# Optimization experiments

Hardware: AMD Instinct MI355X
Metric: run time of the kernel (lower is better)

## Reference

```python
import jax, jax.numpy as jnp
import numpy as np

B, L, D, H = 4, 2048, 1024, 16
HD = D // H  # head_dim = 64


def setup_inputs() -> dict:
    key = jax.random.key(0)
    ks = jax.random.split(key, 13)
    s = 1.0 / np.sqrt(D)
    inp = {
        'q': jax.random.normal(ks[0], (B, L, D), jnp.float32),
        'k': jax.random.normal(ks[1], (B, L, D), jnp.float32),
        'v': jax.random.normal(ks[2], (B, L, D), jnp.float32),
        'mask': jax.random.randint(ks[3], (B, 1, L, L), 0, 2, jnp.int32),
        'WQ': jax.random.normal(ks[4], (D, D), jnp.float32) * s,
        'bQ': jnp.zeros((D,), jnp.float32),
        'WK': jax.random.normal(ks[5], (D, D), jnp.float32) * s,
        'bK': jnp.zeros((D,), jnp.float32),
        'WV': jax.random.normal(ks[6], (D, D), jnp.float32) * s,
        'bV': jnp.zeros((D,), jnp.float32),
        'WO': jax.random.normal(ks[7], (D, D), jnp.float32) * s,
        'bO': jnp.zeros((D,), jnp.float32),
    }
    return inp


def reference(q, k, v, mask, WQ, bQ, WK, bK, WV, bV, WO, bO):
    # Linear projections (torch Linear: x @ W.T + b; here W stored as [D,D], use x @ W + b equivalently)
    Q = q @ WQ + bQ  # [B, L, D]
    K = k @ WK + bK
    V = v @ WV + bV
    # split heads -> [B, H, L, HD]
    Q = Q.reshape(B, L, H, HD).transpose(0, 2, 1, 3)
    K = K.reshape(B, L, H, HD).transpose(0, 2, 1, 3)
    V = V.reshape(B, L, H, HD).transpose(0, 2, 1, 3)
    scale = 1.0 / np.sqrt(HD).astype(np.float32)
    scores = jnp.einsum('bhqd,bhkd->bhqk', Q, K) * scale  # [B, H, Lq, Lk]
    scores = jnp.where(mask == 0, -jnp.inf, scores)  # mask broadcasts over heads
    attn = jax.nn.softmax(scores, axis=-1)
    # dropout p=0 (eval) -> identity
    ctx = jnp.einsum('bhqk,bhkd->bhqd', attn, V)  # [B, H, L, HD]
    ctx = ctx.transpose(0, 2, 1, 3).reshape(B, L, D)
    return ctx @ WO + bO
```

## Files before the change

kernel.cpp:

```cpp
#include <hip/hip_runtime.h>
#include <math.h>

#define B_  4
#define L_  2048
#define D_  1024
#define H_  16
#define HD_ 64

typedef __attribute__((ext_vector_type(8))) short short8;
typedef __attribute__((ext_vector_type(4))) float f32x4;

__device__ static inline unsigned short f2bf(float f) {
    union { float f; unsigned int u; } v; v.f = f;
    const unsigned int u = v.u;
    return (unsigned short)((u + 0x7FFFu + ((u >> 16) & 1u)) >> 16);
}

__device__ static inline void async_copy16(const void* g, void* lds)
{
    __builtin_amdgcn_global_load_lds(
        (const __attribute__((address_space(1))) void*)g,
        (__attribute__((address_space(3))) void*)lds, 16, 0, 0);
}

__global__ __launch_bounds__(256) void cvt_bf16_kernel(
    const float* __restrict__ in, unsigned short* __restrict__ out)
{
    const size_t i = ((size_t)blockIdx.x * 256 + threadIdx.x) * 8;
    const float4 x = *(const float4*)&in[i];
    const float4 y = *(const float4*)&in[i + 4];
    ushort4 o0, o1;
    o0.x = f2bf(x.x); o0.y = f2bf(x.y); o0.z = f2bf(x.z); o0.w = f2bf(x.w);
    o1.x = f2bf(y.x); o1.y = f2bf(y.y); o1.z = f2bf(y.z); o1.w = f2bf(y.w);
    *(ushort4*)&out[i]     = o0;
    *(ushort4*)&out[i + 4] = o1;
}

__global__ __launch_bounds__(256) void transpose_bf16_kernel(
    const float* __restrict__ W, unsigned short* __restrict__ WT)
{
    __shared__ float t[32][33];
    const int c  = threadIdx.x & 31;
    const int r8 = threadIdx.x >> 5;
    const int k0 = blockIdx.y * 32;
    const int n0 = blockIdx.x * 32;
    #pragma unroll
    for (int i = 0; i < 4; ++i) {
        const int r = r8 + i * 8;
        t[r][c] = W[(size_t)(k0 + r) * 1024 + n0 + c];
    }
    __syncthreads();
    #pragma unroll
    for (int i = 0; i < 4; ++i) {
        const int r = r8 + i * 8;
        WT[(size_t)(n0 + r) * 1024 + k0 + c] = f2bf(t[c][r]);
    }
}

__global__ __launch_bounds__(256) void vtrans_kernel(
    const float* __restrict__ Vp, unsigned short* __restrict__ vtb)
{
    __shared__ float t[64][65];
    const int tid = threadIdx.x;
    const int l0  = blockIdx.x * 64;
    const int h   = blockIdx.y;
    const int b   = blockIdx.z;
    const int rr  = tid >> 4;
    const int c4  = (tid & 15) * 4;
    #pragma unroll
    for (int i = 0; i < 4; ++i) {
        const int r = i * 16 + rr;
        const float4 x = *(const float4*)&Vp[((size_t)(b * L_ + l0 + r)) * D_ + h * 64 + c4];
        t[r][c4] = x.x; t[r][c4 + 1] = x.y; t[r][c4 + 2] = x.z; t[r][c4 + 3] = x.w;
    }
    __syncthreads();
    #pragma unroll
    for (int i = 0; i < 4; ++i) {
        const int d = i * 16 + rr;
        ushort4 o;
        o.x = f2bf(t[c4 + 0][d]); o.y = f2bf(t[c4 + 1][d]);
        o.z = f2bf(t[c4 + 2][d]); o.w = f2bf(t[c4 + 3][d]);
        *(ushort4*)&vtb[((size_t)((b * H_ + h) * 64 + d)) * L_ + l0 + c4] = o;
    }
}

__global__ __launch_bounds__(256) void pack_mask_t_kernel(
    const int* __restrict__ mask, unsigned int* __restrict__ mbt)
{
    const unsigned g = blockIdx.x * 256 + threadIdx.x;
    const int v = mask[g];
    const unsigned long long bm = __ballot(v != 0);
    const int lane = threadIdx.x & 63;
    const int b = g >> 22;
    const int q = (g >> 11) & 2047;
    const int k = g & 2047;
    const unsigned idx = ((unsigned)(b * 32 + (k >> 6)) * 2048 + q) * 2 + ((k >> 5) & 1);
    if (lane == 0)       mbt[idx] = (unsigned)bm;
    else if (lane == 32) mbt[idx] = (unsigned)(bm >> 32);
}

__global__ __launch_bounds__(256) void gemm_mfma_kernel(
    const unsigned short* __restrict__ A, const unsigned short* __restrict__ WT,
    const float* __restrict__ bias, float* __restrict__ C,
    int M, int N, int K)
{
    __shared__ __align__(16) unsigned short At[128 * 64];
    __shared__ __align__(16) unsigned short Bt[128 * 64];

    const int tid  = threadIdx.x;
    const int lane = tid & 63;
    const int wave = tid >> 6;
    const int wm   = wave >> 1;
    const int wn   = wave & 1;
    const int quad = lane >> 4;
    const int l15  = lane & 15;
    const int m0   = blockIdx.y * 128;
    const int n0   = blockIdx.x * 128;

    f32x4 acc[4][4];
    #pragma unroll
    for (int i = 0; i < 4; ++i)
        #pragma unroll
        for (int j = 0; j < 4; ++j) acc[i][j] = (f32x4)0.f;

    for (int k0 = 0; k0 < K; k0 += 64) {
        __syncthreads();
        #pragma unroll
        for (int i = 0; i < 4; ++i) {
            const int fb  = i * 256 + wave * 64;
            const int f   = fb + lane;
            const int row = f >> 3;
            const int c8  = f & 7;
            async_copy16(&A [(size_t)(m0 + row) * K + k0 + c8 * 8],
                         (char*)At + (size_t)fb * 16);
            async_copy16(&WT[(size_t)(n0 + row) * K + k0 + c8 * 8],
                         (char*)Bt + (size_t)fb * 16);
        }
        __syncthreads();

        #pragma unroll
        for (int kk = 0; kk < 64; kk += 32) {
            short8 afr[4], bfr[4];
            #pragma unroll
            for (int mt = 0; mt < 4; ++mt)
                afr[mt] = *(const short8*)&At[(size_t)(wm * 64 + mt * 16 + l15) * 64 + kk + quad * 8];
            #pragma unroll
            for (int nt = 0; nt < 4; ++nt)
                bfr[nt] = *(const short8*)&Bt[(size_t)(wn * 64 + nt * 16 + l15) * 64 + kk + quad * 8];
            #pragma unroll
            for (int mt = 0; mt < 4; ++mt)
                #pragma unroll
                for (int nt = 0; nt < 4; ++nt)
                    acc[mt][nt] = __builtin_amdgcn_mfma_f32_16x16x32_bf16(
                        afr[mt], bfr[nt], acc[mt][nt], 0, 0, 0);
        }
    }

    #pragma unroll
    for (int nt = 0; nt < 4; ++nt) {
        const int col = n0 + wn * 64 + nt * 16 + l15;
        const float bv = bias[col];
        #pragma unroll
        for (int mt = 0; mt < 4; ++mt) {
            const int r0 = m0 + wm * 64 + mt * 16 + quad * 4;
            #pragma unroll
            for (int r = 0; r < 4; ++r)
                C[(size_t)(r0 + r) * N + col] = acc[mt][nt][r] + bv;
        }
    }
}

#define AQ 128
#define AK 64
#define PSTR 72

__global__ __launch_bounds__(256) void attn_mfma_kernel(
    const unsigned short* __restrict__ Qb,
    const unsigned short* __restrict__ Kb,
    const unsigned short* __restrict__ Vtg,
    const unsigned int* __restrict__ mbt,
    unsigned short* __restrict__ Cb)
{
    __shared__ __align__(16) unsigned short Kt[AK * 64];
    __shared__ __align__(16) unsigned short Vs[64 * AK];
    __shared__ __align__(16) unsigned short Pt[AQ * PSTR];
    __shared__ __align__(16) unsigned long long Mt[AQ];

    const int tid  = threadIdx.x;
    const int lane = tid & 63;
    const int w    = tid >> 6;
    const int quad = lane >> 4;
    const int l15  = lane & 15;
    const int q0   = blockIdx.x * AQ;
    const int h    = blockIdx.y;
    const int b    = blockIdx.z;

    const float scale = 0.125f * 1.44269504088896340736f;

    short8 qf[2][2];
    #pragma unroll
    for (int qc = 0; qc < 2; ++qc)
        #pragma unroll
        for (int kc = 0; kc < 2; ++kc)
            qf[qc][kc] = *(const short8*)
                &Qb[((size_t)(b * L_ + q0 + w * 32 + qc * 16 + l15)) * D_
                    + h * 64 + kc * 32 + quad * 8];

    f32x4 ot[4][2];
    #pragma unroll
    for (int dr = 0; dr < 4; ++dr)
        #pragma unroll
        for (int qc = 0; qc < 2; ++qc) ot[dr][qc] = (f32x4)0.f;
    float m_run[2] = {-INFINITY, -INFINITY};
    float l_run[2] = {0.f, 0.f};

    for (int kt = 0; kt < L_ / AK; ++kt) {
        const int k0 = kt * AK;
        __syncthreads();
        #pragma unroll
        for (int i = 0; i < 2; ++i) {
            const int fb = i * 256 + w * 64;
            const int f  = fb + lane;
            const int r  = f >> 3;
            const int c8 = f & 7;
            async_copy16(&Kb[((size_t)(b * L_ + k0 + r)) * D_ + h * 64 + c8 * 8],
                         (char*)Kt + fb * 16);
            async_copy16(&Vtg[((size_t)((b * H_ + h) * 64 + r)) * L_ + k0 + c8 * 8],
                         (char*)Vs + fb * 16);
        }
        if (w == 3)
            async_copy16((const char*)mbt + ((size_t)(b * 32 + kt) * L_ + q0) * 8
                             + lane * 16,
                         (char*)Mt);
        __syncthreads();

        f32x4 st[4][2];
        #pragma unroll
        for (int kr = 0; kr < 4; ++kr)
            #pragma unroll
            for (int qc = 0; qc < 2; ++qc) st[kr][qc] = (f32x4)0.f;
        #pragma unroll
        for (int kc = 0; kc < 2; ++kc) {
            short8 kf[4];
            #pragma unroll
            for (int kr = 0; kr < 4; ++kr)
                kf[kr] = *(const short8*)&Kt[(kr * 16 + l15) * 64 + kc * 32 + quad * 8];
            #pragma unroll
            for (int kr = 0; kr < 4; ++kr)
                #pragma unroll
                for (int qc = 0; qc < 2; ++qc)
                    st[kr][qc] = __builtin_amdgcn_mfma_f32_16x16x32_bf16(
                        kf[kr], qf[qc][kc], st[kr][qc], 0, 0, 0);
        }

        #pragma unroll
        for (int qc = 0; qc < 2; ++qc) {
            const unsigned long long mrow = Mt[w * 32 + qc * 16 + l15];
            float rmax = -INFINITY;
            #pragma unroll
            for (int kr = 0; kr < 4; ++kr) {
                const unsigned nib = (unsigned)(mrow >> (kr * 16 + quad * 4)) & 0xFu;
                #pragma unroll
                for (int r = 0; r < 4; ++r) {
                    const float x = ((nib >> r) & 1u) ? st[kr][qc][r] * scale
                                                      : -INFINITY;
                    st[kr][qc][r] = x;
                    rmax = fmaxf(rmax, x);
                }
            }
            rmax = fmaxf(rmax, __shfl_xor(rmax, 16));
            rmax = fmaxf(rmax, __shfl_xor(rmax, 32));
            const float mnew  = fmaxf(m_run[qc], rmax);
            const float msafe = fmaxf(mnew, -1e30f);
            const float alpha = exp2f(m_run[qc] - msafe);
            float psum = 0.f;
            #pragma unroll
            for (int kr = 0; kr < 4; ++kr) {
                const float p0 = exp2f(st[kr][qc][0] - msafe);
                const float p1 = exp2f(st[kr][qc][1] - msafe);
                const float p2 = exp2f(st[kr][qc][2] - msafe);
                const float p3 = exp2f(st[kr][qc][3] - msafe);
                psum += (p0 + p1) + (p2 + p3);
                ushort4 pk;
                pk.x = f2bf(p0); pk.y = f2bf(p1); pk.z = f2bf(p2); pk.w = f2bf(p3);
                *(ushort4*)&Pt[(w * 32 + qc * 16 + l15) * PSTR + kr * 16 + quad * 4] = pk;
            }
            psum += __shfl_xor(psum, 16);
            psum += __shfl_xor(psum, 32);
            l_run[qc] = l_run[qc] * alpha + psum;
            m_run[qc] = mnew;
            #pragma unroll
            for (int dr = 0; dr < 4; ++dr) {
                ot[dr][qc][0] *= alpha; ot[dr][qc][1] *= alpha;
                ot[dr][qc][2] *= alpha; ot[dr][qc][3] *= alpha;
            }
        }

        #pragma unroll
        for (int kc = 0; kc < 2; ++kc) {
            short8 vf[4], pf[2];
            #pragma unroll
            for (int dr = 0; dr < 4; ++dr)
                vf[dr] = *(const short8*)&Vs[(dr * 16 + l15) * 64 + kc * 32 + quad * 8];
            #pragma unroll
            for (int qc = 0; qc < 2; ++qc)
                pf[qc] = *(const short8*)&Pt[(w * 32 + qc * 16 + l15) * PSTR
                                             + kc * 32 + quad * 8];
            #pragma unroll
            for (int dr = 0; dr < 4; ++dr)
                #pragma unroll
                for (int qc = 0; qc < 2; ++qc)
                    ot[dr][qc] = __builtin_amdgcn_mfma_f32_16x16x32_bf16(
                        vf[dr], pf[qc], ot[dr][qc], 0, 0, 0);
        }
    }

    #pragma unroll
    for (int qc = 0; qc < 2; ++qc) {
        const float rinv = (l_run[qc] > 0.f) ? (1.f / l_run[qc]) : 0.f;
        const size_t base = ((size_t)(b * L_ + q0 + w * 32 + qc * 16 + l15)) * D_
                            + h * 64;
        #pragma unroll
        for (int dr = 0; dr < 4; ++dr) {
            ushort4 o;
            o.x = f2bf(ot[dr][qc][0] * rinv);
            o.y = f2bf(ot[dr][qc][1] * rinv);
            o.z = f2bf(ot[dr][qc][2] * rinv);
            o.w = f2bf(ot[dr][qc][3] * rinv);
            *(ushort4*)&Cb[base + dr * 16 + quad * 4] = o;
        }
    }
}

extern "C" void kernel_launch(void* const* d_in, const int* in_sizes, int n_in,
                              void* d_out, int out_size, void* d_ws, size_t ws_size,
                              hipStream_t stream)
{
    const float* q    = (const float*)d_in[0];
    const float* k    = (const float*)d_in[1];
    const float* v    = (const float*)d_in[2];
    const int*   mask = (const int*)d_in[3];
    const float* WQ   = (const float*)d_in[4];
    const float* bQ   = (const float*)d_in[5];
    const float* WK   = (const float*)d_in[6];
    const float* bK   = (const float*)d_in[7];
    const float* WV   = (const float*)d_in[8];
    const float* bV   = (const float*)d_in[9];
    const float* WO   = (const float*)d_in[10];
    const float* bO   = (const float*)d_in[11];
    float* out = (float*)d_out;

    const size_t NTOK = (size_t)B_ * L_;

    char* W = (char*)d_ws;
    float* Qp = (float*)(W);
    float* Kp = (float*)(W + ((size_t)32 << 20));
    float* Vp = (float*)(W + ((size_t)64 << 20));
    unsigned short* qb  = (unsigned short*)(W + ((size_t)96  << 20));
    unsigned short* vb  = (unsigned short*)(W + ((size_t)112 << 20));
    unsigned short* cb  = (unsigned short*)(W);
    unsigned short* WTo = (unsigned short*)(W + ((size_t)32 << 20));

    unsigned int*   mbt = (unsigned int*)d_out;
    unsigned short* WTq = (unsigned short*)((char*)d_out + ((size_t)2 << 20));
    unsigned short* WTk = (unsigned short*)((char*)d_out + ((size_t)4 << 20));
    unsigned short* WTv = (unsigned short*)((char*)d_out + ((size_t)6 << 20));
    unsigned short* kb  = (unsigned short*)((char*)d_out + ((size_t)8 << 20));

    pack_mask_t_kernel<<<(B_ * L_ * L_) / 256, 256, 0, stream>>>(mask, mbt);

    const int cvtg = (int)(NTOK * D_ / (256 * 8));
    cvt_bf16_kernel<<<cvtg, 256, 0, stream>>>(q, qb);
    cvt_bf16_kernel<<<cvtg, 256, 0, stream>>>(k, kb);
    cvt_bf16_kernel<<<cvtg, 256, 0, stream>>>(v, vb);

    dim3 tg(32, 32);
    transpose_bf16_kernel<<<tg, 256, 0, stream>>>(WQ, WTq);
    transpose_bf16_kernel<<<tg, 256, 0, stream>>>(WK, WTk);
    transpose_bf16_kernel<<<tg, 256, 0, stream>>>(WV, WTv);

    dim3 ggrd(D_ / 128, NTOK / 128);
    gemm_mfma_kernel<<<ggrd, 256, 0, stream>>>(qb, WTq, bQ, Qp, (int)NTOK, D_, D_);
    gemm_mfma_kernel<<<ggrd, 256, 0, stream>>>(kb, WTk, bK, Kp, (int)NTOK, D_, D_);
    gemm_mfma_kernel<<<ggrd, 256, 0, stream>>>(vb, WTv, bV, Vp, (int)NTOK, D_, D_);

    cvt_bf16_kernel<<<cvtg, 256, 0, stream>>>(Qp, qb);
    cvt_bf16_kernel<<<cvtg, 256, 0, stream>>>(Kp, kb);
    vtrans_kernel<<<dim3(L_ / 64, H_, B_), 256, 0, stream>>>(Vp, vb);

    dim3 agrd(L_ / AQ, H_, B_);
    attn_mfma_kernel<<<agrd, 256, 0, stream>>>(qb, kb, vb, mbt, cb);

    transpose_bf16_kernel<<<tg, 256, 0, stream>>>(WO, WTo);
    gemm_mfma_kernel<<<ggrd, 256, 0, stream>>>(cb, WTo, bO, out, (int)NTOK, D_, D_);
}
```

Measured before the change: 572.2 us.

## Emit bf16 from projection GEMMs, fold scale, swizzle LDS, lazy softmax rescale

The QKV projection GEMMs now write bf16 directly, with the softmax scale folded into Q. This removes the fp32 intermediate buffers and the separate conversion kernels, and the V transpose now works on bf16. The attention kernel XOR-swizzles the K/V tiles in LDS to avoid bank conflicts. It also uses a 16-bit per-quad mask layout, packs bf16 with v_cvt_pk_bf16_f32, and only rescales the running output when the max grows by more than 8. The lazy rescale trades exactness of the running max for fewer multiplies, which risks overflow margins only in extreme cases.

```diff
diff --git a/kernel.cpp b/kernel.cpp
--- a/kernel.cpp
+++ b/kernel.cpp
@@ -14,6 +14,12 @@
     union { float f; unsigned int u; } v; v.f = f;
     const unsigned int u = v.u;
     return (unsigned short)((u + 0x7FFFu + ((u >> 16) & 1u)) >> 16);
+}
+
+__device__ static inline unsigned cvt_pk_bf16(float a, float b) {
+    unsigned r;
+    asm("v_cvt_pk_bf16_f32 %0, %1, %2" : "=v"(r) : "v"(a), "v"(b));
+    return r;
 }
 
 __device__ static inline void async_copy16(const void* g, void* lds)
@@ -57,10 +63,10 @@
     }
 }
 
-__global__ __launch_bounds__(256) void vtrans_kernel(
-    const float* __restrict__ Vp, unsigned short* __restrict__ vtb)
-{
-    __shared__ float t[64][65];
+__global__ __launch_bounds__(256) void vtrans_bf16_kernel(
+    const unsigned short* __restrict__ Vb, unsigned short* __restrict__ vtb)
+{
+    __shared__ unsigned short t[64][68];
     const int tid = threadIdx.x;
     const int l0  = blockIdx.x * 64;
     const int h   = blockIdx.y;
@@ -70,39 +76,44 @@
     #pragma unroll
     for (int i = 0; i < 4; ++i) {
         const int r = i * 16 + rr;
-        const float4 x = *(const float4*)&Vp[((size_t)(b * L_ + l0 + r)) * D_ + h * 64 + c4];
-        t[r][c4] = x.x; t[r][c4 + 1] = x.y; t[r][c4 + 2] = x.z; t[r][c4 + 3] = x.w;
+        *(ushort4*)&t[r][c4] =
+            *(const ushort4*)&Vb[((size_t)(b * L_ + l0 + r)) * D_ + h * 64 + c4];
     }
     __syncthreads();
     #pragma unroll
     for (int i = 0; i < 4; ++i) {
         const int d = i * 16 + rr;
         ushort4 o;
-        o.x = f2bf(t[c4 + 0][d]); o.y = f2bf(t[c4 + 1][d]);
-        o.z = f2bf(t[c4 + 2][d]); o.w = f2bf(t[c4 + 3][d]);
+        o.x = t[c4 + 0][d]; o.y = t[c4 + 1][d];
+        o.z = t[c4 + 2][d]; o.w = t[c4 + 3][d];
         *(ushort4*)&vtb[((size_t)((b * H_ + h) * 64 + d)) * L_ + l0 + c4] = o;
     }
 }
 
-__global__ __launch_bounds__(256) void pack_mask_t_kernel(
-    const int* __restrict__ mask, unsigned int* __restrict__ mbt)
+__global__ __launch_bounds__(256) void pack_mask16_kernel(
+    const int* __restrict__ mask, unsigned short* __restrict__ mbt)
 {
     const unsigned g = blockIdx.x * 256 + threadIdx.x;
     const int v = mask[g];
     const unsigned long long bm = __ballot(v != 0);
     const int lane = threadIdx.x & 63;
-    const int b = g >> 22;
-    const int q = (g >> 11) & 2047;
-    const int k = g & 2047;
-    const unsigned idx = ((unsigned)(b * 32 + (k >> 6)) * 2048 + q) * 2 + ((k >> 5) & 1);
-    if (lane == 0)       mbt[idx] = (unsigned)bm;
-    else if (lane == 32) mbt[idx] = (unsigned)(bm >> 32);
-}
-
+    if (lane < 4) {
+        const int b  = g >> 22;
+        const int q  = (g >> 11) & 2047;
+        const int kt = (g >> 6) & 31;
+        unsigned long long x = (bm >> (4 * lane)) & 0x000F000F000F000FULL;
+        x |= x >> 12;
+        x |= x >> 24;
+        mbt[((size_t)(b * 32 + kt) * 2048 + q) * 4 + lane] =
+            (unsigned short)(x & 0xFFFFu);
+    }
+}
+
+template<int OUT_BF16>
 __global__ __launch_bounds__(256) void gemm_mfma_kernel(
     const unsigned short* __restrict__ A, const unsigned short* __restrict__ WT,
-    const float* __restrict__ bias, float* __restrict__ C,
-    int M, int N, int K)
+    const float* __restrict__ bias, void* __restrict__ Cv,
+    int M, int N, int K, float omul)
 {
     __shared__ __align__(16) unsigned short At[128 * 64];
     __shared__ __align__(16) unsigned short Bt[128 * 64];
@@ -164,8 +175,13 @@
         for (int mt = 0; mt < 4; ++mt) {
             const int r0 = m0 + wm * 64 + mt * 16 + quad * 4;
             #pragma unroll
-            for (int r = 0; r < 4; ++r)
-                C[(size_t)(r0 + r) * N + col] = acc[mt][nt][r] + bv;
+            for (int r = 0; r < 4; ++r) {
+                const float val = (acc[mt][nt][r] + bv) * omul;
+                if constexpr (OUT_BF16)
+                    ((unsigned short*)Cv)[(size_t)(r0 + r) * N + col] = f2bf(val);
+                else
+                    ((float*)Cv)[(size_t)(r0 + r) * N + col] = val;
+            }
         }
     }
 }
@@ -178,13 +194,13 @@
     const unsigned short* __restrict__ Qb,
     const unsigned short* __restrict__ Kb,
     const unsigned short* __restrict__ Vtg,
-    const unsigned int* __restrict__ mbt,
+    const unsigned short* __restrict__ mbt,
     unsigned short* __restrict__ Cb)
 {
     __shared__ __align__(16) unsigned short Kt[AK * 64];
     __shared__ __align__(16) unsigned short Vs[64 * AK];
     __shared__ __align__(16) unsigned short Pt[AQ * PSTR];
-    __shared__ __align__(16) unsigned long long Mt[AQ];
+    __shared__ __align__(16) unsigned short Mt[AQ * 4];
 
     const int tid  = threadIdx.x;
     const int lane = tid & 63;
@@ -195,8 +211,6 @@
     const int h    = blockIdx.y;
     const int b    = blockIdx.z;
 
-    const float scale = 0.125f * 1.44269504088896340736f;
-
     short8 qf[2][2];
     #pragma unroll
     for (int qc = 0; qc < 2; ++qc)
@@ -222,57 +236,74 @@
             const int fb = i * 256 + w * 64;
             const int f  = fb + lane;
             const int r  = f >> 3;
-            const int c8 = f & 7;
-            async_copy16(&Kb[((size_t)(b * L_ + k0 + r)) * D_ + h * 64 + c8 * 8],
+            const int cs = (f & 7) ^ (r & 7);
+            async_copy16(&Kb[((size_t)(b * L_ + k0 + r)) * D_ + h * 64 + cs * 8],
                          (char*)Kt + fb * 16);
-            async_copy16(&Vtg[((size_t)((b * H_ + h) * 64 + r)) * L_ + k0 + c8 * 8],
+            async_copy16(&Vtg[((size_t)((b * H_ + h) * 64 + r)) * L_ + k0 + cs * 8],
                          (char*)Vs + fb * 16);
         }
         if (w == 3)
-            async_copy16((const char*)mbt + ((size_t)(b * 32 + kt) * L_ + q0) * 8
-                             + lane * 16,
+            async_copy16(&mbt[((size_t)(b * 32 + kt) * 2048 + q0) * 4 + lane * 8],
                          (char*)Mt);
         __syncthreads();
 
         f32x4 st[4][2];
-        #pragma unroll
-        for (int kr = 0; kr < 4; ++kr)
-            #pragma unroll
-            for (int qc = 0; qc < 2; ++qc) st[kr][qc] = (f32x4)0.f;
-        #pragma unroll
-        for (int kc = 0; kc < 2; ++kc) {
+        {
             short8 kf[4];
             #pragma unroll
             for (int kr = 0; kr < 4; ++kr)
-                kf[kr] = *(const short8*)&Kt[(kr * 16 + l15) * 64 + kc * 32 + quad * 8];
+                kf[kr] = *(const short8*)
+                    &Kt[(kr * 16 + l15) * 64 + ((quad ^ (l15 & 7)) * 8)];
             #pragma unroll
             for (int kr = 0; kr < 4; ++kr)
                 #pragma unroll
                 for (int qc = 0; qc < 2; ++qc)
                     st[kr][qc] = __builtin_amdgcn_mfma_f32_16x16x32_bf16(
-                        kf[kr], qf[qc][kc], st[kr][qc], 0, 0, 0);
+                        kf[kr], qf[qc][0], (f32x4)0.f, 0, 0, 0);
+        }
+        {
+            short8 kf[4];
+            #pragma unroll
+            for (int kr = 0; kr < 4; ++kr)
+                kf[kr] = *(const short8*)
+                    &Kt[(kr * 16 + l15) * 64 + (((4 + quad) ^ (l15 & 7)) * 8)];
+            #pragma unroll
+            for (int kr = 0; kr < 4; ++kr)
+                #pragma unroll
+                for (int qc = 0; qc < 2; ++qc)
+                    st[kr][qc] = __builtin_amdgcn_mfma_f32_16x16x32_bf16(
+                        kf[kr], qf[qc][1], st[kr][qc], 0, 0, 0);
         }
 
         #pragma unroll
         for (int qc = 0; qc < 2; ++qc) {
-            const unsigned long long mrow = Mt[w * 32 + qc * 16 + l15];
+            const unsigned m16 = Mt[(w * 32 + qc * 16 + l15) * 4 + quad];
             float rmax = -INFINITY;
             #pragma unroll
             for (int kr = 0; kr < 4; ++kr) {
-                const unsigned nib = (unsigned)(mrow >> (kr * 16 + quad * 4)) & 0xFu;
+                const unsigned nib = (m16 >> (kr * 4)) & 0xFu;
                 #pragma unroll
                 for (int r = 0; r < 4; ++r) {
-                    const float x = ((nib >> r) & 1u) ? st[kr][qc][r] * scale
-                                                      : -INFINITY;
+                    const float x = ((nib >> r) & 1u) ? st[kr][qc][r] : -INFINITY;
                     st[kr][qc][r] = x;
                     rmax = fmaxf(rmax, x);
                 }
             }
             rmax = fmaxf(rmax, __shfl_xor(rmax, 16));
             rmax = fmaxf(rmax, __shfl_xor(rmax, 32));
-            const float mnew  = fmaxf(m_run[qc], rmax);
-            const float msafe = fmaxf(mnew, -1e30f);
-            const float alpha = exp2f(m_run[qc] - msafe);
+            if (__any(rmax > m_run[qc] + 8.f)) {
+                const float mnew  = fmaxf(m_run[qc], rmax);
+                const float msafe = fmaxf(mnew, -1e30f);
+                const float alpha = exp2f(m_run[qc] - msafe);
+                l_run[qc] *= alpha;
+                #pragma unroll
+                for (int dr = 0; dr < 4; ++dr) {
+                    ot[dr][qc][0] *= alpha; ot[dr][qc][1] *= alpha;
+                    ot[dr][qc][2] *= alpha; ot[dr][qc][3] *= alpha;
+                }
+                m_run[qc] = mnew;
+            }
+            const float msafe = fmaxf(m_run[qc], -1e30f);
             float psum = 0.f;
             #pragma unroll
             for (int kr = 0; kr < 4; ++kr) {
@@ -281,19 +312,14 @@
                 const float p2 = exp2f(st[kr][qc][2] - msafe);
                 const float p3 = exp2f(st[kr][qc][3] - msafe);
                 psum += (p0 + p1) + (p2 + p3);
-                ushort4 pk;
-                pk.x = f2bf(p0); pk.y = f2bf(p1); pk.z = f2bf(p2); pk.w = f2bf(p3);
-                *(ushort4*)&Pt[(w * 32 + qc * 16 + l15) * PSTR + kr * 16 + quad * 4] = pk;
+                uint2 pk;
+                pk.x = cvt_pk_bf16(p0, p1);
+                pk.y = cvt_pk_bf16(p2, p3);
+                *(uint2*)&Pt[(w * 32 + qc * 16 + l15) * PSTR + kr * 16 + quad * 4] = pk;
             }
             psum += __shfl_xor(psum, 16);
             psum += __shfl_xor(psum, 32);
-            l_run[qc] = l_run[qc] * alpha + psum;
-            m_run[qc] = mnew;
-            #pragma unroll
-            for (int dr = 0; dr < 4; ++dr) {
-                ot[dr][qc][0] *= alpha; ot[dr][qc][1] *= alpha;
-                ot[dr][qc][2] *= alpha; ot[dr][qc][3] *= alpha;
-            }
+            l_run[qc] += psum;
         }
 
         #pragma unroll
@@ -301,7 +327,8 @@
             short8 vf[4], pf[2];
             #pragma unroll
             for (int dr = 0; dr < 4; ++dr)
-                vf[dr] = *(const short8*)&Vs[(dr * 16 + l15) * 64 + kc * 32 + quad * 8];
+                vf[dr] = *(const short8*)
+                    &Vs[(dr * 16 + l15) * 64 + (((kc * 4 + quad) ^ (l15 & 7)) * 8)];
             #pragma unroll
             for (int qc = 0; qc < 2; ++qc)
                 pf[qc] = *(const short8*)&Pt[(w * 32 + qc * 16 + l15) * PSTR
@@ -353,44 +380,44 @@
     const size_t NTOK = (size_t)B_ * L_;
 
     char* W = (char*)d_ws;
-    float* Qp = (float*)(W);
-    float* Kp = (float*)(W + ((size_t)32 << 20));
-    float* Vp = (float*)(W + ((size_t)64 << 20));
-    unsigned short* qb  = (unsigned short*)(W + ((size_t)96  << 20));
-    unsigned short* vb  = (unsigned short*)(W + ((size_t)112 << 20));
-    unsigned short* cb  = (unsigned short*)(W);
-    unsigned short* WTo = (unsigned short*)(W + ((size_t)32 << 20));
-
-    unsigned int*   mbt = (unsigned int*)d_out;
+    unsigned short* qin = (unsigned short*)(W);
+    unsigned short* kin = (unsigned short*)(W + ((size_t)16  << 20));
+    unsigned short* vin = (unsigned short*)(W + ((size_t)32  << 20));
+    unsigned short* qbf = (unsigned short*)(W + ((size_t)48  << 20));
+    unsigned short* kbf = (unsigned short*)(W + ((size_t)64  << 20));
+    unsigned short* vbf = (unsigned short*)(W + ((size_t)80  << 20));
+    unsigned short* vtb = (unsigned short*)(W + ((size_t)96  << 20));
+    unsigned short* cb  = (unsigned short*)(W + ((size_t)112 << 20));
+    unsigned short* WTo = vin;
+
+    unsigned short* mbt16 = (unsigned short*)d_out;
     unsigned short* WTq = (unsigned short*)((char*)d_out + ((size_t)2 << 20));
     unsigned short* WTk = (unsigned short*)((char*)d_out + ((size_t)4 << 20));
     unsigned short* WTv = (unsigned short*)((char*)d_out + ((size_t)6 << 20));
-    unsigned short* kb  = (unsigned short*)((char*)d_out + ((size_t)8 << 20));
-
-    pack_mask_t_kernel<<<(B_ * L_ * L_) / 256, 256, 0, stream>>>(mask, mbt);
+
+    pack_mask16_kernel<<<(B_ * L_ * L_) / 256, 256, 0, stream>>>(mask, mbt16);
 
     const int cvtg = (int)(NTOK * D_ / (256 * 8));
-    cvt_bf16_kernel<<<cvtg, 256, 0, stream>>>(q, qb);
-    cvt_bf16_kernel<<<cvtg, 256, 0, stream>>>(k, kb);
-    cvt_bf16_kernel<<<cvtg, 256, 0, stream>>>(v, vb);
+    cvt_bf16_kernel<<<cvtg, 256, 0, stream>>>(q, qin);
+    cvt_bf16_kernel<<<cvtg, 256, 0, stream>>>(k, kin);
+    cvt_bf16_kernel<<<cvtg, 256, 0, stream>>>(v, vin);
 
     dim3 tg(32, 32);
     transpose_bf16_kernel<<<tg, 256, 0, stream>>>(WQ, WTq);
     transpose_bf16_kernel<<<tg, 256, 0, stream>>>(WK, WTk);
     transpose_bf16_kernel<<<tg, 256, 0, stream>>>(WV, WTv);
 
+    const float qscale = 0.125f * 1.44269504088896340736f;
     dim3 ggrd(D_ / 128, NTOK / 128);
-    gemm_mfma_kernel<<<ggrd, 256, 0, stream>>>(qb, WTq, bQ, Qp, (int)NTOK, D_, D_);
-    gemm_mfma_kernel<<<ggrd, 256, 0, stream>>>(kb, WTk, bK, Kp, (int)NTOK, D_, D_);
-    gemm_mfma_kernel<<<ggrd, 256, 0, stream>>>(vb, WTv, bV, Vp, (int)NTOK, D_, D_);
-
-    cvt_bf16_kernel<<<cvtg, 256, 0, stream>>>(Qp, qb);
-    cvt_bf16_kernel<<<cvtg, 256, 0, stream>>>(Kp, kb);
-    vtrans_kernel<<<dim3(L_ / 64, H_, B_), 256, 0, stream>>>(Vp, vb);
+    gemm_mfma_kernel<1><<<ggrd, 256, 0, stream>>>(qin, WTq, bQ, qbf, (int)NTOK, D_, D_, qscale);
+    gemm_mfma_kernel<1><<<ggrd, 256, 0, stream>>>(kin, WTk, bK, kbf, (int)NTOK, D_, D_, 1.f);
+    gemm_mfma_kernel<1><<<ggrd, 256, 0, stream>>>(vin, WTv, bV, vbf, (int)NTOK, D_, D_, 1.f);
+
+    transpose_bf16_kernel<<<tg, 256, 0, stream>>>(WO, WTo);
+    vtrans_bf16_kernel<<<dim3(L_ / 64, H_, B_), 256, 0, stream>>>(vbf, vtb);
 
     dim3 agrd(L_ / AQ, H_, B_);
-    attn_mfma_kernel<<<agrd, 256, 0, stream>>>(qb, kb, vb, mbt, cb);
-
-    transpose_bf16_kernel<<<tg, 256, 0, stream>>>(WO, WTo);
-    gemm_mfma_kernel<<<ggrd, 256, 0, stream>>>(cb, WTo, bO, out, (int)NTOK, D_, D_);
-}
+    attn_mfma_kernel<<<agrd, 256, 0, stream>>>(qbf, kbf, vtb, mbt16, cb);
+
+    gemm_mfma_kernel<0><<<ggrd, 256, 0, stream>>>(cb, WTo, bO, out, (int)NTOK, D_, D_, 1.f);
+}
```

Result: faster. 533.9 us (-6.7%).
